# Optimization experiments

Hardware: AMD Instinct MI355X
Metric: run time of the kernel (lower is better)

## Reference

```python
import jax, jax.numpy as jnp
import numpy as np

PARTITION_LENGTH = 64
NUM_PARTITIONS = 1024
BATCH = 2048


def setup_inputs() -> dict:
    key = jax.random.key(0)
    x = jax.random.normal(key, (BATCH, NUM_PARTITIONS * PARTITION_LENGTH), dtype=jnp.float32)
    return {"x": x}


def reference(x) -> jnp.ndarray:
    # Each nn.Linear(partition_length, 1, bias=False) has weight fixed to ones,
    # so it is a sum over a contiguous partition of the feature dim.
    B = x.shape[0]
    # [B, P*L] -> [B, P, L] -> sum over L -> [B, P]
    return x.reshape(B, NUM_PARTITIONS, PARTITION_LENGTH).sum(axis=-1)
```

## Files before the change

### kernel.cpp

```cpp
#include <hip/hip_runtime.h>
#include <hip/hip_bf16.h>


__global__ __launch_bounds__(256) void PartialSum_85478439125876_kernel(
    const float4* __restrict__ x4, float* __restrict__ out, long long n4) {
    long long tid = (long long)blockIdx.x * blockDim.x + threadIdx.x;
    if (tid >= n4) return;

    float4 v = x4[tid];
    float s = v.x + v.y + v.z + v.w;

    s += __shfl_xor(s, 1, 64);
    s += __shfl_xor(s, 2, 64);
    s += __shfl_xor(s, 4, 64);
    s += __shfl_xor(s, 8, 64);

    if ((threadIdx.x & 15) == 0) {
        out[tid >> 4] = s;
    }
}

extern "C" void kernel_launch(void* const* d_in, const int* in_sizes, int n_in,
                              void* d_out, int out_size, void* d_ws, size_t ws_size,
                              hipStream_t stream) {
    const float* x = (const float*)d_in[0];
    float* out = (float*)d_out;

    long long n = (long long)in_sizes[0];
    long long n4 = n / 4;

    const int BLOCK = 256;
    long long grid = (n4 + BLOCK - 1) / BLOCK;

    PartialSum_85478439125876_kernel<<<(unsigned)grid, BLOCK, 0, stream>>>(
        (const float4*)x, out, n4);
}
```

Baseline: 654.4 us.

## Use grid-stride loop with eight independent vector loads per thread

Replaces the one-float4-per-thread launch with a capped persistent grid of up to 2048 blocks. Each thread processes eight strided float4 chunks per iteration, issuing all loads before reducing. The aim is to raise memory-level parallelism and cut block scheduling overhead for this bandwidth-bound reduction. A tail loop handles leftovers; the reduced grid could underfill the device if it is too small.

New measurement: 696.3 us. 1.06x slower.

```diff
diff --git a/kernel.cpp b/kernel.cpp
--- a/kernel.cpp
+++ b/kernel.cpp
@@ -1,22 +1,41 @@
 #include <hip/hip_runtime.h>
-#include <hip/hip_bf16.h>
 
 
+typedef float f4 __attribute__((ext_vector_type(4)));
+
 __global__ __launch_bounds__(256) void PartialSum_85478439125876_kernel(
-    const float4* __restrict__ x4, float* __restrict__ out, long long n4) {
-    long long tid = (long long)blockIdx.x * blockDim.x + threadIdx.x;
-    if (tid >= n4) return;
+    const f4* __restrict__ x4, float* __restrict__ out, long long n4) {
+    const long long stride = (long long)gridDim.x * blockDim.x;
+    long long i = (long long)blockIdx.x * blockDim.x + threadIdx.x;
+    const bool writer = (threadIdx.x & 15) == 0;
 
-    float4 v = x4[tid];
-    float s = v.x + v.y + v.z + v.w;
+    for (; i + 7 * stride < n4; i += 8 * stride) {
+        f4 v[8];
+#pragma unroll
+        for (int j = 0; j < 8; ++j) v[j] = x4[i + j * stride];
 
-    s += __shfl_xor(s, 1, 64);
-    s += __shfl_xor(s, 2, 64);
-    s += __shfl_xor(s, 4, 64);
-    s += __shfl_xor(s, 8, 64);
+        float s[8];
+#pragma unroll
+        for (int j = 0; j < 8; ++j) s[j] = (v[j].x + v[j].y) + (v[j].z + v[j].w);
 
-    if ((threadIdx.x & 15) == 0) {
-        out[tid >> 4] = s;
+#pragma unroll
+        for (int m = 1; m < 16; m <<= 1) {
+#pragma unroll
+            for (int j = 0; j < 8; ++j) s[j] += __shfl_xor(s[j], m, 64);
+        }
+
+        if (writer) {
+#pragma unroll
+            for (int j = 0; j < 8; ++j) out[(i + j * stride) >> 4] = s[j];
+        }
+    }
+
+    for (; i < n4; i += stride) {
+        f4 v = x4[i];
+        float s = (v.x + v.y) + (v.z + v.w);
+#pragma unroll
+        for (int m = 1; m < 16; m <<= 1) s += __shfl_xor(s, m, 64);
+        if (writer) out[i >> 4] = s;
     }
 }
 
@@ -30,8 +49,9 @@
     long long n4 = n / 4;
 
     const int BLOCK = 256;
-    long long grid = (n4 + BLOCK - 1) / BLOCK;
+    long long maxg = (n4 + BLOCK - 1) / BLOCK;
+    int grid = (int)(maxg < 2048 ? maxg : 2048);
 
-    PartialSum_85478439125876_kernel<<<(unsigned)grid, BLOCK, 0, stream>>>(
-        (const float4*)x, out, n4);
+    PartialSum_85478439125876_kernel<<<grid, BLOCK, 0, stream>>>(
+        (const f4*)x, out, n4);
 }
```

## Assign one thread per partition with nontemporal vector loads and stores

Applied to the files above, without the earlier changes.

Each thread now sums an entire 64-float partition with sixteen 16-byte nontemporal loads and writes one output directly, replacing the per-float4 thread mapping and cross-lane shuffle reduction. This removes the shuffles and the masked store and gives each thread more independent loads in flight. In exchange, adjacent lanes access addresses 256 bytes apart per load instruction, which can reduce coalescing efficiency, and the nontemporal hints change cache behaviour.

After: 838.6 us. 28.1% more time.

```diff
diff --git a/kernel.cpp b/kernel.cpp
--- a/kernel.cpp
+++ b/kernel.cpp
@@ -1,23 +1,31 @@
 #include <hip/hip_runtime.h>
-#include <hip/hip_bf16.h>
 
 
+typedef float f4 __attribute__((ext_vector_type(4)));
+
 __global__ __launch_bounds__(256) void PartialSum_85478439125876_kernel(
-    const float4* __restrict__ x4, float* __restrict__ out, long long n4) {
-    long long tid = (long long)blockIdx.x * blockDim.x + threadIdx.x;
-    if (tid >= n4) return;
+    const f4* __restrict__ x4, float* __restrict__ out, long long npart) {
+    long long p = (long long)blockIdx.x * blockDim.x + threadIdx.x;
+    if (p >= npart) return;
 
-    float4 v = x4[tid];
-    float s = v.x + v.y + v.z + v.w;
+    const f4* b = x4 + (p << 4);
 
-    s += __shfl_xor(s, 1, 64);
-    s += __shfl_xor(s, 2, 64);
-    s += __shfl_xor(s, 4, 64);
-    s += __shfl_xor(s, 8, 64);
+    f4 a0 = __builtin_nontemporal_load(b + 0);
+    f4 a1 = __builtin_nontemporal_load(b + 1);
+    f4 a2 = __builtin_nontemporal_load(b + 2);
+    f4 a3 = __builtin_nontemporal_load(b + 3);
+#pragma unroll
+    for (int l = 1; l < 4; ++l) {
+        a0 += __builtin_nontemporal_load(b + l * 4 + 0);
+        a1 += __builtin_nontemporal_load(b + l * 4 + 1);
+        a2 += __builtin_nontemporal_load(b + l * 4 + 2);
+        a3 += __builtin_nontemporal_load(b + l * 4 + 3);
+    }
 
-    if ((threadIdx.x & 15) == 0) {
-        out[tid >> 4] = s;
-    }
+    f4 t = (a0 + a1) + (a2 + a3);
+    float s = (t.x + t.y) + (t.z + t.w);
+
+    __builtin_nontemporal_store(s, out + p);
 }
 
 extern "C" void kernel_launch(void* const* d_in, const int* in_sizes, int n_in,
@@ -27,11 +35,11 @@
     float* out = (float*)d_out;
 
     long long n = (long long)in_sizes[0];
-    long long n4 = n / 4;
+    long long npart = n / 64;
 
     const int BLOCK = 256;
-    long long grid = (n4 + BLOCK - 1) / BLOCK;
+    long long grid = (npart + BLOCK - 1) / BLOCK;
 
     PartialSum_85478439125876_kernel<<<(unsigned)grid, BLOCK, 0, stream>>>(
-        (const float4*)x, out, n4);
+        (const f4*)x, out, npart);
 }
```
